# Optimization experiments

Hardware: AMD Instinct MI355X
Metric: run time of the kernel (lower is better)

Reference implementation:

```python
import jax, jax.numpy as jnp
import numpy as np

E = 256

def setup_inputs() -> dict:
    key = jax.random.key(0)
    ks = jax.random.split(key, 10)
    N, T_y, T_x = 8, 300, 160
    s = 1.0 / np.sqrt(E)  # torch-style uniform-ish init scale, keeps gates unsaturated
    return {
        "inputs": jax.random.normal(ks[0], (N, T_y, E // 2), jnp.float32),
        "memory": jax.random.normal(ks[1], (N, T_x, E), jnp.float32),
        "h0": jnp.zeros((1, N, E), jnp.float32),
        "Wih": jax.random.normal(ks[2], (3 * E, E // 2), jnp.float32) * s,
        "Whh": jax.random.normal(ks[3], (3 * E, E), jnp.float32) * s,
        "bih": jax.random.normal(ks[4], (3 * E,), jnp.float32) * s,
        "bhh": jax.random.normal(ks[5], (3 * E,), jnp.float32) * s,
        "W": jax.random.normal(ks[6], (E, E), jnp.float32) * s,
        "U": jax.random.normal(ks[7], (E, E), jnp.float32) * s,
        "v": jax.random.normal(ks[8], (E,), jnp.float32) * s,
    }


def reference(inputs, memory, h0, Wih, Whh, bih, bhh, W, U, v):
    # GRU (PyTorch gate order r, z, n), batch_first, single layer, unidirectional.
    def step(h, x_t):
        gi = x_t @ Wih.T + bih      # [N, 3E]
        gh = h @ Whh.T + bhh        # [N, 3E]
        ir, iz, i_n = jnp.split(gi, 3, axis=-1)
        hr, hz, hn = jnp.split(gh, 3, axis=-1)
        r = jax.nn.sigmoid(ir + hr)
        z = jax.nn.sigmoid(iz + hz)
        n = jnp.tanh(i_n + r * hn)
        h_new = (1.0 - z) * n + z * h
        return h_new, h_new

    h_last, outs = jax.lax.scan(step, h0[0], jnp.swapaxes(inputs, 0, 1))
    outputs = jnp.swapaxes(outs, 0, 1)   # [N, T_y, E]
    hidden = h_last[None]                # [1, N, E]

    # Bahdanau additive attention
    w = outputs @ W.T                    # [N, T_y, E]
    u = memory @ U.T                     # [N, T_x, E]
    # scores: v . tanh(w + u) broadcast over [N, T_y, T_x, E]
    scores = jnp.einsum('ntxe,e->ntx', jnp.tanh(w[:, :, None, :] + u[:, None, :, :]), v)
    attn_weights = jax.nn.softmax(scores, axis=2)  # [N, T_y, T_x]
    return attn_weights, outputs, hidden
```

## Files before the change

### kernel.cpp

```cpp
#include <hip/hip_runtime.h>


typedef _Float16 f16x2 __attribute__((ext_vector_type(2)));
typedef _Float16 f16x8 __attribute__((ext_vector_type(8)));
typedef float f32x4 __attribute__((ext_vector_type(4)));

__device__ __forceinline__ float fexp2(float x) { return __builtin_amdgcn_exp2f(x); }
__device__ __forceinline__ float frcp(float x) { return __builtin_amdgcn_rcpf(x); }
__device__ __forceinline__ float fsig(float x) {
    return frcp(1.0f + fexp2(x * -1.4426950408889634f));
}
__device__ __forceinline__ float ftanh(float x) {
    return 1.0f - 2.0f * frcp(1.0f + fexp2(x * 2.8853900817779268f));
}

__device__ __forceinline__ float pick4(f32x4 v, int s) {
    float ab = (s & 1) ? v[1] : v[0];
    float cd = (s & 1) ? v[3] : v[2];
    return (s & 2) ? cd : ab;
}

#define FLAG(i) ((i) * 32)

__global__ __launch_bounds__(256) void phase1_kernel(
    const float* __restrict__ Whh, unsigned* __restrict__ wd,
    const float* __restrict__ inputs, const float* __restrict__ Wih,
    float* __restrict__ gi, const float* __restrict__ bih,
    const float* __restrict__ bhh, int* flags, int full) {
    if (full && blockIdx.x == 0 && threadIdx.x < 9)
        flags[FLAG(threadIdx.x)] = 0;
    if (blockIdx.x < 384) {
        int gid = blockIdx.x * 256 + threadIdx.x;
        int i = gid >> 9, t = gid & 511;
        int fi = i >> 2, j = i & 3;
        int g = fi >> 4, m2 = (fi >> 3) & 1, ks = fi & 7;
        int w = t >> 6, l = t & 63;
        int row = 256 * g + 32 * w + 16 * m2 + (l & 15);
        int k = 32 * ks + 8 * (l >> 4) + 2 * j;
        union { unsigned u; f16x2 h; } cv;
        cv.h[0] = (_Float16)Whh[(size_t)row * 256 + k];
        cv.h[1] = (_Float16)Whh[(size_t)row * 256 + k + 1];
        wd[i * 512 + t] = cv.u;
        return;
    }
    int id = blockIdx.x - 384;
    const int n0 = (id % 12) * 64, m0 = (id / 12) * 64;
    __shared__ float Xs[32][65];
    __shared__ float Ws2[32][65];
    const int tid = threadIdx.x;
    const int tx = tid & 15, ty = tid >> 4;
    const int M = 2400, K = 128;
    float acc[4][4] = {};
    for (int k0 = 0; k0 < K; k0 += 32) {
#pragma unroll
        for (int i = 0; i < 8; ++i) {
            int e = tid + i * 256;
            int kk = e & 31, m = e >> 5;
            int row = m0 + m;
            Xs[kk][m] = (row < M) ? inputs[(size_t)row * K + k0 + kk] : 0.0f;
            Ws2[kk][m] = Wih[(size_t)(n0 + m) * K + k0 + kk];
        }
        __syncthreads();
#pragma unroll
        for (int kk = 0; kk < 32; ++kk) {
            float a[4], b[4];
#pragma unroll
            for (int i = 0; i < 4; ++i) a[i] = Xs[kk][ty * 4 + i];
#pragma unroll
            for (int j = 0; j < 4; ++j) b[j] = Ws2[kk][tx * 4 + j];
#pragma unroll
            for (int i = 0; i < 4; ++i)
#pragma unroll
                for (int j = 0; j < 4; ++j) acc[i][j] += a[i] * b[j];
        }
        __syncthreads();
    }
#pragma unroll
    for (int i = 0; i < 4; ++i) {
        int row = m0 + ty * 4 + i;
        if (row >= M) continue;
        int b = row / 300;
        int t = row - b * 300;
#pragma unroll
        for (int j = 0; j < 4; ++j) {
            int col = n0 + tx * 4 + j;
            float val = acc[i][j] + ((col < 512) ? (bih[col] + bhh[col]) : bih[col]);
            gi[(size_t)(t * 8 + b) * 768 + col] = val;
        }
    }
}

__global__ __launch_bounds__(256) void gemm_kernel(
    const float* __restrict__ X, const float* __restrict__ Wt,
    float* __restrict__ C, _Float16* __restrict__ C16,
    int M, int N, int K, int mode) {
    __shared__ float Xs[32][65];
    __shared__ float Ws2[32][65];
    const int n0 = blockIdx.x * 64, m0 = blockIdx.y * 64;
    const int tid = threadIdx.x;
    const int tx = tid & 15, ty = tid >> 4;
    float acc[4][4] = {};
    for (int k0 = 0; k0 < K; k0 += 32) {
#pragma unroll
        for (int i = 0; i < 8; ++i) {
            int e = tid + i * 256;
            int kk = e & 31, m = e >> 5;
            int row = m0 + m;
            Xs[kk][m] = (row < M) ? X[(size_t)row * K + k0 + kk] : 0.0f;
            Ws2[kk][m] = Wt[(size_t)(n0 + m) * K + k0 + kk];
        }
        __syncthreads();
#pragma unroll
        for (int kk = 0; kk < 32; ++kk) {
            float a[4], b[4];
#pragma unroll
            for (int i = 0; i < 4; ++i) a[i] = Xs[kk][ty * 4 + i];
#pragma unroll
            for (int j = 0; j < 4; ++j) b[j] = Ws2[kk][tx * 4 + j];
#pragma unroll
            for (int i = 0; i < 4; ++i)
#pragma unroll
                for (int j = 0; j < 4; ++j) acc[i][j] += a[i] * b[j];
        }
        __syncthreads();
    }
#pragma unroll
    for (int i = 0; i < 4; ++i) {
        int row = m0 + ty * 4 + i;
        if (row >= M) continue;
#pragma unroll
        for (int j = 0; j < 4; ++j) {
            int col = n0 + tx * 4 + j;
            if (mode == 2) C16[(size_t)row * N + col] = (_Float16)acc[i][j];
            else           C[(size_t)row * N + col] = acc[i][j];
        }
    }
}

__global__ __launch_bounds__(512, 1) void gru_mega(
    const float* __restrict__ gi, const unsigned* __restrict__ wd,
    const float* __restrict__ h0, const float* __restrict__ bhh,
    float* __restrict__ outs, float* __restrict__ hid,
    const float* __restrict__ memory, const float* __restrict__ Um,
    _Float16* __restrict__ u16, const float* __restrict__ W,
    const float* __restrict__ vv, float* __restrict__ attn,
    int* flags, int full) {
    __shared__ __align__(16) _Float16 hbuf[2][256];
    __shared__ float Xs[32][65];
    __shared__ float Ws2[32][65];
    __shared__ unsigned uS[160 * 129];
    __shared__ __align__(16) float oL[10][260];
    __shared__ float wLf[10][256];
    __shared__ float vL[256], scP[2][160], sc[160], red[2];

    const int tid = threadIdx.x;

    if (blockIdx.x >= 8) {
        int id = blockIdx.x - 8;
        if (id < 80) {
            const int n0 = (id & 3) * 64, m0 = (id >> 2) * 64;
            const int tx = tid & 15, ty = (tid & 255) >> 4;
            float acc[4][4] = {};
            for (int k0 = 0; k0 < 256; k0 += 32) {
                if (tid < 256) {
#pragma unroll
                    for (int i = 0; i < 8; ++i) {
                        int e = tid + i * 256;
                        int kk = e & 31, m = e >> 5;
                        Xs[kk][m] = memory[(size_t)(m0 + m) * 256 + k0 + kk];
                        Ws2[kk][m] = Um[(size_t)(n0 + m) * 256 + k0 + kk];
                    }
                }
                __syncthreads();
                if (tid < 256) {
#pragma unroll
                    for (int kk = 0; kk < 32; ++kk) {
                        float a[4], b[4];
#pragma unroll
                        for (int i = 0; i < 4; ++i) a[i] = Xs[kk][ty * 4 + i];
#pragma unroll
                        for (int j = 0; j < 4; ++j) b[j] = Ws2[kk][tx * 4 + j];
#pragma unroll
                        for (int i = 0; i < 4; ++i)
#pragma unroll
                            for (int j = 0; j < 4; ++j) acc[i][j] += a[i] * b[j];
                    }
                }
                __syncthreads();
            }
            if (tid < 256) {
#pragma unroll
                for (int i = 0; i < 4; ++i)
#pragma unroll
                    for (int j = 0; j < 4; ++j)
                        u16[(size_t)(m0 + ty * 4 + i) * 256 + n0 + tx * 4 + j] =
                            (_Float16)acc[i][j];
            }
            if (!full) return;
            __syncthreads();
            if (tid == 0)
                __hip_atomic_fetch_add(&flags[FLAG(8)], 1, __ATOMIC_RELEASE,
                                       __HIP_MEMORY_SCOPE_AGENT);
        }
        if (!full) return;

        const int grp = id / 30;
        const int tc = id % 30;
        if (tid == 0) {
            while (__hip_atomic_load(&flags[FLAG(8)], __ATOMIC_RELAXED,
                                     __HIP_MEMORY_SCOPE_AGENT) < 80)
                __builtin_amdgcn_s_sleep(64);
            while (__hip_atomic_load(&flags[FLAG(8)], __ATOMIC_ACQUIRE,
                                     __HIP_MEMORY_SCOPE_AGENT) < 80)
                __builtin_amdgcn_s_sleep(8);
        }
        __syncthreads();
        const unsigned* ug = (const unsigned*)(u16 + (size_t)grp * 160 * 256);
        for (int i = tid; i < 20480; i += 512)
            uS[(i >> 7) * 129 + (i & 127)] = ug[i];
        if (tid < 256) vL[tid] = vv[tid];
        __syncthreads();

        if (tid == 0) {
            while (__hip_atomic_load(&flags[FLAG(grp)], __ATOMIC_RELAXED,
                                     __HIP_MEMORY_SCOPE_AGENT) < 1)
                __builtin_amdgcn_s_sleep(127);
            while (__hip_atomic_load(&flags[FLAG(grp)], __ATOMIC_ACQUIRE,
                                     __HIP_MEMORY_SCOPE_AGENT) < 1)
                __builtin_amdgcn_s_sleep(8);
        }
        __syncthreads();
        for (int i = tid; i < 2560; i += 512) {
            int ti = i >> 8, k = i & 255;
            oL[ti][k] = outs[((size_t)grp * 300 + tc * 10 + ti) * 256 + k];
        }
        __syncthreads();
        {
            const int c = tid & 255, rh = tid >> 8;
            float a0 = 0, a1 = 0, a2 = 0, a3 = 0, a4 = 0;
            const float* wr = W + (size_t)c * 256;
            const int r0 = rh * 5;
            for (int k4 = 0; k4 < 256; k4 += 4) {
                float4 wq = *(const float4*)(wr + k4);
#define WROW(ACC, TI)                                                     \
                {                                                         \
                    float4 oq = *(const float4*)(&oL[TI][k4]);            \
                    ACC += wq.x * oq.x + wq.y * oq.y +                    \
                           wq.z * oq.z + wq.w * oq.w;                     \
                }
                WROW(a0, r0 + 0) WROW(a1, r0 + 1) WROW(a2, r0 + 2)
                WROW(a3, r0 + 3) WROW(a4, r0 + 4)
#undef WROW
            }
            wLf[r0 + 0][c] = a0; wLf[r0 + 1][c] = a1; wLf[r0 + 2][c] = a2;
            wLf[r0 + 3][c] = a3; wLf[r0 + 4][c] = a4;
        }
        __syncthreads();
        for (int ti = 0; ti < 10; ++ti) {
            if (tid < 320) {
                const int x = (tid < 160) ? tid : tid - 160;
                const int half = (tid >= 160) ? 1 : 0;
                const unsigned* ur = uS + x * 129 + half * 64;
                const float* wl = wLf[ti] + half * 128;
                const float* vl = vL + half * 128;
                float acc2 = 0.0f;
#pragma unroll 8
                for (int e2 = 0; e2 < 64; ++e2) {
                    union { unsigned uu2; _Float16 hh[2]; } cv;
                    cv.uu2 = ur[e2];
                    int ee = e2 * 2;
                    acc2 += vl[ee] * ftanh(wl[ee] + (float)cv.hh[0]);
                    acc2 += vl[ee + 1] * ftanh(wl[ee + 1] + (float)cv.hh[1]);
                }
                scP[half][x] = acc2;
            }
            __syncthreads();
            if (tid < 160) sc[tid] = scP[0][tid] + scP[1][tid];
            __syncthreads();
            if (tid < 64) {
                float m = -3.0e38f;
                for (int i = tid; i < 160; i += 64) m = fmaxf(m, sc[i]);
#pragma unroll
                for (int o = 32; o; o >>= 1) m = fmaxf(m, __shfl_xor(m, o));
                if (tid == 0) red[0] = m;
            }
            __syncthreads();
            float ee = 0.0f;
            if (tid < 160) {
                ee = fexp2((sc[tid] - red[0]) * 1.4426950408889634f);
                sc[tid] = ee;
            }
            __syncthreads();
            if (tid < 64) {
                float s = 0.0f;
                for (int i = tid; i < 160; i += 64) s += sc[i];
#pragma unroll
                for (int o = 32; o; o >>= 1) s += __shfl_xor(s, o);
                if (tid == 0) red[1] = s;
            }
            __syncthreads();
            if (tid < 160)
                attn[(size_t)(grp * 300 + tc * 10 + ti) * 160 + tid] =
                    ee * frcp(red[1]);
            __syncthreads();
        }
        return;
    }

    const int b = blockIdx.x;
    const int t = tid;
    const int w = t >> 6, l = t & 63;
    const int grp = l >> 4;
    const int sel = l & 7;
    const int hi = (l >> 3) & 1;
    const int m2s = sel >> 2, rsel = sel & 3;
    const int e = 32 * w + 16 * m2s + 4 * grp + rsel;

    f16x8 wf[48];
#pragma unroll
    for (int fi = 0; fi < 48; ++fi) {
        union { unsigned u[4]; f16x8 v; } cv;
#pragma unroll
        for (int j = 0; j < 4; ++j) cv.u[j] = wd[(fi * 4 + j) * 512 + t];
        wf[fi] = cv.v;
    }

    float h = h0[b * 256 + e];
    float bn = bhh[512 + e];
    if (!hi) hbuf[0][e] = (_Float16)h;
    const float* gp = gi + b * 768;
    float* op = outs + (size_t)b * 76800 + e;

    float gr = gp[e], gz = gp[e + 256], gn = gp[e + 512];
    __syncthreads();

    for (int st = 0; st < 300; ++st) {
        int stn = (st < 299) ? st + 1 : st;
        const float* g = gp + (size_t)stn * 6144;
        float grn = g[e], gzn = g[e + 256], gnn = g[e + 512];

        const _Float16* hb = hbuf[st & 1];
        f16x8 hv0 = *(const f16x8*)(hb + 0 * 32 + 8 * grp);
        f16x8 hv1 = *(const f16x8*)(hb + 1 * 32 + 8 * grp);
        f16x8 hv2 = *(const f16x8*)(hb + 2 * 32 + 8 * grp);
        f16x8 hv3 = *(const f16x8*)(hb + 3 * 32 + 8 * grp);
        f16x8 hv4 = *(const f16x8*)(hb + 4 * 32 + 8 * grp);
        f16x8 hv5 = *(const f16x8*)(hb + 5 * 32 + 8 * grp);
        f16x8 hv6 = *(const f16x8*)(hb + 6 * 32 + 8 * grp);
        f16x8 hv7 = *(const f16x8*)(hb + 7 * 32 + 8 * grp);

        f32x4 aR0 = {0.f, 0.f, 0.f, 0.f}, aR1 = {0.f, 0.f, 0.f, 0.f};
        f32x4 aZ0 = {0.f, 0.f, 0.f, 0.f}, aZ1 = {0.f, 0.f, 0.f, 0.f};
        f32x4 aN0 = {0.f, 0.f, 0.f, 0.f}, aN1 = {0.f, 0.f, 0.f, 0.f};
#define KSTEP(ks, hv)                                                        \
        aR0 = __builtin_amdgcn_mfma_f32_16x16x32_f16(wf[0 * 8 + ks], hv, aR0, 0, 0, 0); \
        aR1 = __builtin_amdgcn_mfma_f32_16x16x32_f16(wf[1 * 8 + ks], hv, aR1, 0, 0, 0); \
        aZ0 = __builtin_amdgcn_mfma_f32_16x16x32_f16(wf[2 * 8 + ks], hv, aZ0, 0, 0, 0); \
        aZ1 = __builtin_amdgcn_mfma_f32_16x16x32_f16(wf[3 * 8 + ks], hv, aZ1, 0, 0, 0); \
        aN0 = __builtin_amdgcn_mfma_f32_16x16x32_f16(wf[4 * 8 + ks], hv, aN0, 0, 0, 0); \
        aN1 = __builtin_amdgcn_mfma_f32_16x16x32_f16(wf[5 * 8 + ks], hv, aN1, 0, 0, 0);
        KSTEP(0, hv0) KSTEP(1, hv1) KSTEP(2, hv2) KSTEP(3, hv3)
        KSTEP(4, hv4) KSTEP(5, hv5) KSTEP(6, hv6) KSTEP(7, hv7)
#undef KSTEP

        f32x4 vR = m2s ? aR1 : aR0;
        f32x4 vZ = m2s ? aZ1 : aZ0;
        f32x4 vN = m2s ? aN1 : aN0;
        float sr = pick4(vR, rsel);
        float sz = pick4(vZ, rsel);
        float sn = pick4(vN, rsel);

        float r = fsig(gr + sr);
        float z = fsig(gz + sz);
        float n = ftanh(gn + r * (sn + bn));
        h = n + z * (h - n);

        gr = grn; gz = gzn; gn = gnn;

        if (hi)
            op[st * 256] = h;
        else
            hbuf[(st + 1) & 1][e] = (_Float16)h;
        asm volatile("s_waitcnt lgkmcnt(0)\n\ts_barrier" ::: "memory");
    }
    if (!hi) hid[b * 256 + e] = h;
    if (full) {
        asm volatile("s_waitcnt vmcnt(0)" ::: "memory");
        __syncthreads();
        if (t == 0)
            __hip_atomic_store(&flags[FLAG(b)], 1, __ATOMIC_RELEASE,
                               __HIP_MEMORY_SCOPE_AGENT);
    }
}

__global__ __launch_bounds__(256) void wattn_kernel(
    const _Float16* __restrict__ u16, const float* __restrict__ outs,
    const float* __restrict__ W, const float* __restrict__ vv,
    float* __restrict__ attn) {
    const int tc = blockIdx.x, b = blockIdx.y;
    const int tid = threadIdx.x;
    __shared__ unsigned uS[160 * 129];
    __shared__ __align__(16) float oL[10][260];
    __shared__ float wLf[10][256];
    __shared__ float vL[256], sc[160], red[2];

    const unsigned* ug = (const unsigned*)(u16 + (size_t)b * 160 * 256);
    for (int i = tid; i < 20480; i += 256)
        uS[(i >> 7) * 129 + (i & 127)] = ug[i];
    vL[tid] = vv[tid];
    for (int i = tid; i < 2560; i += 256) {
        int ti = i >> 8, k = i & 255;
        oL[ti][k] = outs[((size_t)b * 300 + tc * 10 + ti) * 256 + k];
    }
    __syncthreads();
    {
        float a0 = 0, a1 = 0, a2 = 0, a3 = 0, a4 = 0;
        float a5 = 0, a6 = 0, a7 = 0, a8 = 0, a9 = 0;
        for (int k4 = 0; k4 < 256; k4 += 4) {
            float4 wq = *(const float4*)(W + (size_t)tid * 256 + k4);
#define WROW(ACC, TI)                                                     \
            {                                                             \
                float4 oq = *(const float4*)(&oL[TI][k4]);                \
                ACC += wq.x * oq.x + wq.y * oq.y +                        \
                       wq.z * oq.z + wq.w * oq.w;                        \
            }
            WROW(a0, 0) WROW(a1, 1) WROW(a2, 2) WROW(a3, 3) WROW(a4, 4)
            WROW(a5, 5) WROW(a6, 6) WROW(a7, 7) WROW(a8, 8) WROW(a9, 9)
#undef WROW
        }
        wLf[0][tid] = a0; wLf[1][tid] = a1; wLf[2][tid] = a2;
        wLf[3][tid] = a3; wLf[4][tid] = a4; wLf[5][tid] = a5;
        wLf[6][tid] = a6; wLf[7][tid] = a7; wLf[8][tid] = a8;
        wLf[9][tid] = a9;
    }
    __syncthreads();
    for (int ti = 0; ti < 10; ++ti) {
        int t = tc * 10 + ti;
        float acc2 = 0.0f;
        if (tid < 160) {
            const unsigned* ur = uS + tid * 129;
            const float* wl = wLf[ti];
#pragma unroll 8
            for (int e2 = 0; e2 < 128; ++e2) {
                union { unsigned uu2; _Float16 hh[2]; } cv;
                cv.uu2 = ur[e2];
                int ee = e2 * 2;
                acc2 += vL[ee] * ftanh(wl[ee] + (float)cv.hh[0]);
                acc2 += vL[ee + 1] * ftanh(wl[ee + 1] + (float)cv.hh[1]);
            }
            sc[tid] = acc2;
        }
        __syncthreads();
        if (tid < 64) {
            float m = -3.0e38f;
            for (int i = tid; i < 160; i += 64) m = fmaxf(m, sc[i]);
#pragma unroll
            for (int o = 32; o; o >>= 1) m = fmaxf(m, __shfl_xor(m, o));
            if (tid == 0) red[0] = m;
        }
        __syncthreads();
        float ee = 0.0f;
        if (tid < 160) {
            ee = fexp2((acc2 - red[0]) * 1.4426950408889634f);
            sc[tid] = ee;
        }
        __syncthreads();
        if (tid < 64) {
            float s = 0.0f;
            for (int i = tid; i < 160; i += 64) s += sc[i];
#pragma unroll
            for (int o = 32; o; o >>= 1) s += __shfl_xor(s, o);
            if (tid == 0) red[1] = s;
        }
        __syncthreads();
        if (tid < 160)
            attn[(size_t)(b * 300 + t) * 160 + tid] = ee * frcp(red[1]);
        __syncthreads();
    }
}

extern "C" void kernel_launch(void* const* d_in, const int* in_sizes, int n_in,
                              void* d_out, int out_size, void* d_ws, size_t ws_size,
                              hipStream_t stream) {
    const float* inputs = (const float*)d_in[0];
    const float* memory = (const float*)d_in[1];
    const float* h0 = (const float*)d_in[2];
    const float* Wih = (const float*)d_in[3];
    const float* Whh = (const float*)d_in[4];
    const float* bih = (const float*)d_in[5];
    const float* bhh = (const float*)d_in[6];
    const float* Wm = (const float*)d_in[7];
    const float* Um = (const float*)d_in[8];
    const float* vv = (const float*)d_in[9];

    float* out = (float*)d_out;
    float* out_attn = out;
    float* out_outputs = out + 384000;
    float* out_hidden = out + 998400;

    char* ws = (char*)d_ws;
    float* gi = (float*)ws;
    unsigned* wd = (unsigned*)(ws + 7372800);

    const size_t U16_OFF = 7766016, FLAG_OFF = 8421376;
    const bool full = ws_size >= FLAG_OFF + 1152;
    _Float16* u16 = full ? (_Float16*)(ws + U16_OFF) : (_Float16*)ws;
    int* flags = (int*)(ws + FLAG_OFF);

    phase1_kernel<<<840, 256, 0, stream>>>(Whh, wd, inputs, Wih, gi, bih, bhh,
                                           flags, full ? 1 : 0);
    if (full) {
        gru_mega<<<248, 512, 0, stream>>>(gi, wd, h0, bhh, out_outputs,
                                          out_hidden, memory, Um, u16, Wm, vv,
                                          out_attn, flags, 1);
    } else {
        gru_mega<<<8, 512, 0, stream>>>(gi, wd, h0, bhh, out_outputs,
                                        out_hidden, memory, Um, u16, Wm, vv,
                                        out_attn, flags, 0);
        gemm_kernel<<<dim3(4, 20), 256, 0, stream>>>(memory, Um, nullptr, u16,
                                                     1280, 256, 256, 2);
        wattn_kernel<<<dim3(30, 8), 256, 0, stream>>>(u16, out_outputs, Wm, vv,
                                                      out_attn);
    }
}
```

Baseline: 464.3 us.

## Publish GRU step progress so attention blocks start on partial outputs

The recurrent kernel now writes the number of completed timesteps into its per-batch flag at a few checkpoints (104, 204, 274, 300) rather than only a done flag at the end. Each attention tile waits only until the timesteps it needs are written, so attention work can overlap the tail of the sequential GRU. Spin loops now poll with atomic RMW adds of zero followed by a single acquire fence instead of a second acquire-load loop. The checkpoints add extra barriers and vmcnt drains inside the serial recurrence, which lengthens the critical path slightly.

```diff
diff --git a/kernel.cpp b/kernel.cpp
--- a/kernel.cpp
+++ b/kernel.cpp
@@ -21,6 +21,15 @@
 }
 
 #define FLAG(i) ((i) * 32)
+
+__device__ __forceinline__ int flag_rmw_relaxed(int* p) {
+    return __hip_atomic_fetch_add(p, 0, __ATOMIC_RELAXED,
+                                  __HIP_MEMORY_SCOPE_AGENT);
+}
+__device__ __forceinline__ void flag_fence_acquire(int* p) {
+    (void)__hip_atomic_fetch_add(p, 0, __ATOMIC_ACQUIRE,
+                                 __HIP_MEMORY_SCOPE_AGENT);
+}
 
 __global__ __launch_bounds__(256) void phase1_kernel(
     const float* __restrict__ Whh, unsigned* __restrict__ wd,
@@ -207,12 +216,9 @@
         const int grp = id / 30;
         const int tc = id % 30;
         if (tid == 0) {
-            while (__hip_atomic_load(&flags[FLAG(8)], __ATOMIC_RELAXED,
-                                     __HIP_MEMORY_SCOPE_AGENT) < 80)
+            while (flag_rmw_relaxed(&flags[FLAG(8)]) < 80)
                 __builtin_amdgcn_s_sleep(64);
-            while (__hip_atomic_load(&flags[FLAG(8)], __ATOMIC_ACQUIRE,
-                                     __HIP_MEMORY_SCOPE_AGENT) < 80)
-                __builtin_amdgcn_s_sleep(8);
+            flag_fence_acquire(&flags[FLAG(8)]);
         }
         __syncthreads();
         const unsigned* ug = (const unsigned*)(u16 + (size_t)grp * 160 * 256);
@@ -221,13 +227,11 @@
         if (tid < 256) vL[tid] = vv[tid];
         __syncthreads();
 
+        const int need = tc * 10 + 10;
         if (tid == 0) {
-            while (__hip_atomic_load(&flags[FLAG(grp)], __ATOMIC_RELAXED,
-                                     __HIP_MEMORY_SCOPE_AGENT) < 1)
+            while (flag_rmw_relaxed(&flags[FLAG(grp)]) < need)
                 __builtin_amdgcn_s_sleep(127);
-            while (__hip_atomic_load(&flags[FLAG(grp)], __ATOMIC_ACQUIRE,
-                                     __HIP_MEMORY_SCOPE_AGENT) < 1)
-                __builtin_amdgcn_s_sleep(8);
+            flag_fence_acquire(&flags[FLAG(grp)]);
         }
         __syncthreads();
         for (int i = tid; i < 2560; i += 512) {
@@ -335,6 +339,13 @@
     __syncthreads();
 
     for (int st = 0; st < 300; ++st) {
+        if (full && (st == 104 || st == 204 || st == 274)) {
+            asm volatile("s_waitcnt vmcnt(0)" ::: "memory");
+            __syncthreads();
+            if (t == 0)
+                __hip_atomic_store(&flags[FLAG(b)], st, __ATOMIC_RELEASE,
+                                   __HIP_MEMORY_SCOPE_AGENT);
+        }
         int stn = (st < 299) ? st + 1 : st;
         const float* g = gp + (size_t)stn * 6144;
         float grn = g[e], gzn = g[e + 256], gnn = g[e + 512];
@@ -388,7 +399,7 @@
         asm volatile("s_waitcnt vmcnt(0)" ::: "memory");
         __syncthreads();
         if (t == 0)
-            __hip_atomic_store(&flags[FLAG(b)], 1, __ATOMIC_RELEASE,
+            __hip_atomic_store(&flags[FLAG(b)], 300, __ATOMIC_RELEASE,
                                __HIP_MEMORY_SCOPE_AGENT);
     }
 }
```

After: 488.1 us. 1.05x slower.
